# Optimization experiments

Measured on AMD Instinct MI355X. Metric: run time of the kernel, lower is better.

## Reference

```python
import jax, jax.numpy as jnp
import numpy as np

B, S, H = 2, 1024, 4096
NH, D = 32, 128
ROPE_BASE = 10000.0
W_BITS, A_BITS = 4, 8


def fake_quant(x, n_bits):
    """Symmetric fake quantization along the last dim (per-token / per-channel)."""
    qmax = 2.0 ** (n_bits - 1) - 1.0
    scale = jnp.max(jnp.abs(x), axis=-1, keepdims=True) / qmax
    scale = jnp.maximum(scale, 1e-8)
    q = jnp.clip(jnp.round(x / scale), -qmax - 1.0, qmax) * scale
    # straight-through estimator (matches fake-quant training semantics)
    return x + jax.lax.stop_gradient(q - x)


def quant_linear(x, w):
    # x: [..., in], w: [out, in]; quantize activation per-token, weight per-out-channel
    xq = fake_quant(x, A_BITS)
    wq = fake_quant(w, W_BITS)
    return jnp.einsum('bsi,oi->bso', xq, wq)


def rope_tables(seq_len, dim, dtype):
    inv_freq = 1.0 / (ROPE_BASE ** (jnp.arange(0, dim, 2, dtype=jnp.float32) / dim))
    t = jnp.arange(seq_len, dtype=jnp.float32)
    freqs = jnp.einsum('i,j->ij', t, inv_freq)          # [S, D/2]
    emb = jnp.concatenate([freqs, freqs], axis=-1)       # [S, D]
    return jnp.cos(emb).astype(dtype), jnp.sin(emb).astype(dtype)


def rotate_half(x):
    x1, x2 = jnp.split(x, 2, axis=-1)
    return jnp.concatenate([-x2, x1], axis=-1)


def setup_inputs() -> dict:
    key = jax.random.key(0)
    ks = jax.random.split(key, 5)
    hidden_states = jax.random.normal(ks[0], (B, S, H), jnp.float32)
    wq = jax.random.normal(ks[1], (H, H), jnp.float32) * 0.02
    wk = jax.random.normal(ks[2], (H, H), jnp.float32) * 0.02
    wv = jax.random.normal(ks[3], (H, H), jnp.float32) * 0.02
    wo = jax.random.normal(ks[4], (H, H), jnp.float32) * 0.02
    return {"hidden_states": hidden_states, "wq": wq, "wk": wk, "wv": wv, "wo": wo}


def reference(hidden_states, wq, wk, wv, wo):
    bsz, q_len, _ = hidden_states.shape
    # quantized QKV projections
    q = quant_linear(hidden_states, wq).reshape(bsz, q_len, NH, D).transpose(0, 2, 1, 3)
    k = quant_linear(hidden_states, wk).reshape(bsz, q_len, NH, D).transpose(0, 2, 1, 3)
    v = quant_linear(hidden_states, wv).reshape(bsz, q_len, NH, D).transpose(0, 2, 1, 3)
    # RoPE
    cos, sin = rope_tables(q_len, D, hidden_states.dtype)   # [S, D]
    cos = cos[None, None, :, :]
    sin = sin[None, None, :, :]
    q = q * cos + rotate_half(q) * sin
    k = k * cos + rotate_half(k) * sin
    # quantized QK^T
    qq = fake_quant(q, A_BITS)
    kq = fake_quant(k, A_BITS)
    scores = jnp.einsum('bhqd,bhkd->bhqk', qq, kq) / jnp.sqrt(jnp.float32(D))
    # causal mask
    causal = jnp.tril(jnp.ones((q_len, q_len), dtype=bool))
    scores = jnp.where(causal[None, None], scores, jnp.finfo(scores.dtype).min)
    p = jax.nn.softmax(scores, axis=-1)
    # quantized PV
    pq = fake_quant(p, A_BITS)
    vq = fake_quant(v, A_BITS)
    attn = jnp.einsum('bhqk,bhkd->bhqd', pq, vq)
    attn = attn.transpose(0, 2, 1, 3).reshape(bsz, q_len, H)
    # quantized output projection
    return quant_linear(attn, wo)
```

## Files before the change

kernel.cpp:

```cpp
#include <hip/hip_runtime.h>
#include <stdint.h>

#define S_LEN 1024
#define HDIM  4096
#define NHEAD 32
#define DHEAD 128
#define BATCH 2
#define MTOK  (BATCH * S_LEN)

typedef __attribute__((ext_vector_type(4))) int   i32x4;
typedef __attribute__((ext_vector_type(4))) float f32x4;
typedef __attribute__((ext_vector_type(8))) short bf16x8;

#define GLOBAL_AS __attribute__((address_space(1)))
#define LDS_AS    __attribute__((address_space(3)))

__device__ __forceinline__ void gl2lds16(const void* g, void* l) {
  __builtin_amdgcn_global_load_lds((const GLOBAL_AS unsigned int*)(g),
                                   (LDS_AS unsigned int*)(l), 16, 0, 0);
}

__device__ __forceinline__ unsigned short f2bf(float f) {
  unsigned int u = __float_as_uint(f);
  unsigned int r = (u + 0x7fffu + ((u >> 16) & 1u)) >> 16;
  return (unsigned short)r;
}

__global__ __launch_bounds__(256) void rowquant_kernel(
    const float* __restrict__ x, int8_t* __restrict__ q,
    float* __restrict__ scales, float qmax, float clipLo)
{
  const int row = blockIdx.x;
  const int t = threadIdx.x;
  const float* xr = x + (size_t)row * HDIM;
  float4 v[4];
  float am = 0.f;
#pragma unroll
  for (int i = 0; i < 4; ++i) {
    v[i] = ((const float4*)xr)[t + 256 * i];
    am = fmaxf(am, fmaxf(fmaxf(fabsf(v[i].x), fabsf(v[i].y)),
                         fmaxf(fabsf(v[i].z), fabsf(v[i].w))));
  }
#pragma unroll
  for (int off = 32; off > 0; off >>= 1) am = fmaxf(am, __shfl_down(am, off));
  __shared__ float wred[4];
  if ((t & 63) == 0) wred[t >> 6] = am;
  __syncthreads();
  const float m = fmaxf(fmaxf(wred[0], wred[1]), fmaxf(wred[2], wred[3]));
  const float scale = fmaxf(m / qmax, 1e-8f);
  if (t == 0) scales[row] = scale;
  int* qo = (int*)(q + (size_t)row * HDIM);
#pragma unroll
  for (int i = 0; i < 4; ++i) {
    int b0 = (int)fminf(fmaxf(rintf(v[i].x / scale), clipLo), qmax);
    int b1 = (int)fminf(fmaxf(rintf(v[i].y / scale), clipLo), qmax);
    int b2 = (int)fminf(fmaxf(rintf(v[i].z / scale), clipLo), qmax);
    int b3 = (int)fminf(fmaxf(rintf(v[i].w / scale), clipLo), qmax);
    qo[t + 256 * i] = (b0 & 0xff) | ((b1 & 0xff) << 8) | ((b2 & 0xff) << 16) | ((b3 & 0xff) << 24);
  }
}

__global__ __launch_bounds__(256) void ropetab_kernel(
    float* __restrict__ ct, float* __restrict__ st)
{
  const int t = blockIdx.x * 256 + threadIdx.x;
  const int s = t >> 6, d = t & 63;
  const float inv = powf(10000.0f, -(float)d * (1.0f / 64.0f));
  const float ang = (float)s * inv;
  float sn, c;
  sincosf(ang, &sn, &c);
  ct[t] = c;
  st[t] = sn;
}

template<int MODE>
__global__ __launch_bounds__(256, 2) void gemm_i8_fused_kernel(
    const int8_t* __restrict__ A, const float* __restrict__ sa,
    const int8_t* __restrict__ Bw, const float* __restrict__ sb,
    float* __restrict__ C,
    int8_t* __restrict__ o8, float* __restrict__ oscale,
    const float* __restrict__ ctab, const float* __restrict__ stab,
    unsigned short* __restrict__ vqT)
{
  __shared__ __align__(16) char smem[128 * 129 * 4];
  __shared__ float vscale[128];
  int8_t (*asB)[128 * 128] = (int8_t(*)[128 * 128])smem;
  int8_t (*bsB)[128 * 128] = (int8_t(*)[128 * 128])(smem + 32768);
  float (*fx)[129] = (float(*)[129])smem;

  const int flat = blockIdx.y * gridDim.x + blockIdx.x;
  const int nf = (flat & 7) * 64 + (flat >> 3);
  const int bmi = nf & 15, bni = nf >> 4;
  const int bm = bmi * 128, bn = bni * 128;

  const int tid = threadIdx.x;
  const int w = tid >> 6, l = tid & 63;
  const int l15 = l & 15, lg = l >> 4, l7 = l & 7;
  const int lr = l >> 3, g7 = l & 7;
  const int m0 = (w >> 1) * 64, n0 = (w & 1) * 64;

  const int8_t* aT = A + (size_t)(bm + lr) * HDIM + ((g7 ^ lr) << 4);
  const int8_t* bT = Bw + (size_t)(bn + lr) * HDIM + ((g7 ^ lr) << 4);

  i32x4 acc[4][4];
#pragma unroll
  for (int i = 0; i < 4; ++i)
#pragma unroll
    for (int j = 0; j < 4; ++j) acc[i][j] = (i32x4){0, 0, 0, 0};

  auto stage = [&](int t) {
    const int bf = t & 1;
    const size_t k = (size_t)t * 128;
#pragma unroll
    for (int i = 0; i < 4; ++i) {
      const int r0 = w * 32 + i * 8;
      gl2lds16(aT + (size_t)r0 * HDIM + k, asB[bf] + r0 * 128);
      gl2lds16(bT + (size_t)r0 * HDIM + k, bsB[bf] + r0 * 128);
    }
  };

  stage(0);
  asm volatile("s_waitcnt vmcnt(0)" ::: "memory");
  __builtin_amdgcn_s_barrier();

  for (int t = 0; t < 32; ++t) {
    if (t < 31) stage(t + 1);
    const int cur = t & 1;
    __builtin_amdgcn_s_setprio(1);
#pragma unroll
    for (int kk = 0; kk < 2; ++kk) {
      i32x4 aF[4], bF[4];
      const int slot = (((kk << 2) + lg) ^ l7) << 4;
#pragma unroll
      for (int i = 0; i < 4; ++i)
        aF[i] = *(const i32x4*)(asB[cur] + (m0 + i * 16 + l15) * 128 + slot);
#pragma unroll
      for (int j = 0; j < 4; ++j)
        bF[j] = *(const i32x4*)(bsB[cur] + (n0 + j * 16 + l15) * 128 + slot);
#pragma unroll
      for (int i = 0; i < 4; ++i)
#pragma unroll
        for (int j = 0; j < 4; ++j)
          acc[i][j] = __builtin_amdgcn_mfma_i32_16x16x64_i8(aF[i], bF[j], acc[i][j], 0, 0, 0);
    }
    __builtin_amdgcn_s_setprio(0);
    if (t < 31) {
      asm volatile("s_waitcnt vmcnt(0)" ::: "memory");
      __builtin_amdgcn_s_barrier();
    }
  }

  float sbr[4];
#pragma unroll
  for (int j = 0; j < 4; ++j) sbr[j] = sb[bn + n0 + j * 16 + l15];

  if (MODE == 0) {
#pragma unroll
    for (int i = 0; i < 4; ++i) {
#pragma unroll
      for (int r = 0; r < 4; ++r) {
        const int m = bm + m0 + i * 16 + lg * 4 + r;
        const float sm = sa[m];
        float* cp = C + (size_t)m * HDIM + bn + n0 + l15;
#pragma unroll
        for (int j = 0; j < 4; ++j)
          cp[j * 16] = sm * sbr[j] * (float)acc[i][j][r];
      }
    }
    return;
  }

  __syncthreads();
#pragma unroll
  for (int i = 0; i < 4; ++i) {
#pragma unroll
    for (int r = 0; r < 4; ++r) {
      const int ml = m0 + i * 16 + lg * 4 + r;
      const float sm = sa[bm + ml];
#pragma unroll
      for (int j = 0; j < 4; ++j)
        fx[ml][n0 + j * 16 + l15] = sm * sbr[j] * (float)acc[i][j][r];
    }
  }
  __syncthreads();

  const int h = bn >> 7;

  if (MODE == 1) {
    const int row = tid >> 1, half = tid & 1;
    const int sg = bm + row;
    const int b = sg >> 10, s = sg & (S_LEN - 1);
    const float* ct = ctab + (size_t)s * 64;
    const float* st = stab + (size_t)s * 64;
    float am = 0.f;
#pragma unroll
    for (int d0 = 0; d0 < 64; ++d0) {
      const int d = half * 64 + d0;
      const float x0 = fx[row][d];
      const float x1 = fx[row][d ^ 64];
      const float c = ct[d0], sn = st[d0];
      const float v = half ? (x0 * c + x1 * sn) : (x0 * c - x1 * sn);
      fx[row][d] = v;
      am = fmaxf(am, fabsf(v));
    }
    am = fmaxf(am, __shfl_xor(am, 1));
    const float scale = fmaxf(am * (1.0f / 127.0f), 1e-8f);
    int8_t* op = o8 + (((size_t)(b * NHEAD + h)) * S_LEN + s) * DHEAD + half * 64;
#pragma unroll
    for (int c4 = 0; c4 < 4; ++c4) {
      i32x4 dw;
#pragma unroll
      for (int u = 0; u < 4; ++u) {
        int pk = 0;
#pragma unroll
        for (int bi = 0; bi < 4; ++bi) {
          const float v = fx[row][half * 64 + c4 * 16 + u * 4 + bi];
          const int q = (int)fminf(fmaxf(rintf(v / scale), -128.f), 127.f);
          pk |= (q & 0xff) << (8 * bi);
        }
        dw[u] = pk;
      }
      *(i32x4*)(op + c4 * 16) = dw;
    }
    if (!half) oscale[((size_t)(b * NHEAD + h)) * S_LEN + s] = scale;
  } else {
    {
      const int row = tid >> 1, half = tid & 1;
      float am = 0.f;
#pragma unroll
      for (int d0 = 0; d0 < 64; ++d0)
        am = fmaxf(am, fabsf(fx[row][half * 64 + d0]));
      am = fmaxf(am, __shfl_xor(am, 1));
      if (!half) vscale[row] = fmaxf(am * (1.0f / 127.0f), 1e-8f);
    }
    __syncthreads();
    {
      const int d = tid >> 1, sh = tid & 1;
      const int b = bm >> 10;
      const int bh = b * NHEAD + h;
      unsigned short* op = vqT + ((size_t)bh * DHEAD + d) * S_LEN + (bm & (S_LEN - 1)) + sh * 64;
#pragma unroll
      for (int c8 = 0; c8 < 8; ++c8) {
        i32x4 dw;
#pragma unroll
        for (int u = 0; u < 4; ++u) {
          const int sl = sh * 64 + c8 * 8 + u * 2;
          const float sc0 = vscale[sl], sc1 = vscale[sl + 1];
          const float q0 = fminf(fmaxf(rintf(fx[sl][d] / sc0), -128.f), 127.f);
          const float q1 = fminf(fmaxf(rintf(fx[sl + 1][d] / sc1), -128.f), 127.f);
          dw[u] = (int)f2bf(q0 * sc0) | ((int)f2bf(q1 * sc1) << 16);
        }
        *(i32x4*)(op + c8 * 8) = dw;
      }
    }
  }
}

#define QB 64
#define KB 64

__global__ __launch_bounds__(256) void attn_mfma_kernel(
    const int8_t* __restrict__ qq, const float* __restrict__ sq,
    const int8_t* __restrict__ kq, const float* __restrict__ sk,
    const unsigned short* __restrict__ vqT,
    float* __restrict__ attn)
{
  __shared__ __align__(16) int8_t ks[KB * 128];
  __shared__ __align__(16) unsigned short vs[128 * 64];
  __shared__ __align__(16) unsigned short ps[QB][64];
  __shared__ float sk_t[KB];

  const int tid = threadIdx.x;
  const int w = tid >> 6;
  const int l = tid & 63;
  const int l15 = l & 15;
  const int lg = l >> 4;
  const int lr = l >> 3, g7 = l & 7;
  const int bflat = blockIdx.x;
  const int bh = (bflat & 7) + 8 * (bflat >> 6);
  const int qxb = (bflat >> 3) & 7;
  const size_t bhS = (size_t)bh * S_LEN;
  const int b = bh >> 5, h = bh & 31;
  const int NT = S_LEN / QB;

  for (int rep = 0; rep < 2; ++rep) {
    const int qt = rep ? (NT - 1 - qxb) : qxb;
    const int q0 = qt * QB;
    const int nkt = qt + 1;

    const int qrow = q0 + w * 16 + l15;
    const int8_t* qp = qq + (bhS + qrow) * (size_t)DHEAD;
    const i32x4 qa0 = *(const i32x4*)(qp + lg * 16);
    const i32x4 qa1 = *(const i32x4*)(qp + 64 + lg * 16);

    float sqv[4];
    int qg[4];
#pragma unroll
    for (int r = 0; r < 4; ++r) {
      qg[r] = q0 + w * 16 + lg * 4 + r;
      sqv[r] = sq[bhS + qg[r]] * 0.08838834764831843f * 1.4426950408889634f;
    }

    float m_run[4] = {-3.0e38f, -3.0e38f, -3.0e38f, -3.0e38f};
    float rs[4] = {0.f, 0.f, 0.f, 0.f};
    f32x4 oacc[8];
#pragma unroll
    for (int ds = 0; ds < 8; ++ds) oacc[ds] = (f32x4){0.f, 0.f, 0.f, 0.f};

    const int qloc = w * 16 + l15;
    const int swA0 = (lg ^ (qloc & 7)) << 3;
    const int swA1 = ((lg + 4) ^ (qloc & 7)) << 3;

    for (int kt = 0; kt < nkt; ++kt) {
      const int k0 = kt * KB;
#pragma unroll
      for (int i = 0; i < 2; ++i) {
        const int r0 = w * 16 + i * 8;
        gl2lds16(kq + (bhS + k0 + r0 + lr) * (size_t)128 + ((g7 ^ lr) << 4),
                 ks + r0 * 128);
      }
#pragma unroll
      for (int i = 0; i < 4; ++i) {
        const int r0 = w * 32 + i * 8;
        const unsigned short* src = vqT + ((size_t)bh * 128 + r0 + lr) * S_LEN
                                        + k0 + ((g7 ^ lr) << 3);
        gl2lds16(src, vs + r0 * 64);
      }
      if (tid < KB) sk_t[tid] = sk[bhS + k0 + tid];
      __syncthreads();
      const bool diag = (kt == nkt - 1);

      float s2v[4][4];
      float tmax[4] = {-3.0e38f, -3.0e38f, -3.0e38f, -3.0e38f};
#pragma unroll
      for (int c = 0; c < 4; ++c) {
        const int krow = c * 16 + l15;
        const i32x4 b0 = *(const i32x4*)(ks + krow * 128 + ((lg ^ (krow & 7)) << 4));
        const i32x4 b1 = *(const i32x4*)(ks + krow * 128 + (((lg + 4) ^ (krow & 7)) << 4));
        i32x4 acc = {0, 0, 0, 0};
        acc = __builtin_amdgcn_mfma_i32_16x16x64_i8(qa0, b0, acc, 0, 0, 0);
        acc = __builtin_amdgcn_mfma_i32_16x16x64_i8(qa1, b1, acc, 0, 0, 0);
        const float skv = sk_t[krow];
        const int kgl = k0 + krow;
#pragma unroll
        for (int r = 0; r < 4; ++r) {
          const bool valid = !diag || (kgl <= qg[r]);
          const float s2 = valid ? ((float)acc[r] * sqv[r] * skv) : -3.0e38f;
          s2v[c][r] = s2;
          tmax[r] = fmaxf(tmax[r], s2);
        }
      }
#pragma unroll
      for (int r = 0; r < 4; ++r)
#pragma unroll
        for (int off = 1; off < 16; off <<= 1)
          tmax[r] = fmaxf(tmax[r], __shfl_xor(tmax[r], off));

#pragma unroll
      for (int r = 0; r < 4; ++r) {
        const float m_new = fmaxf(m_run[r], tmax[r]);
        const float f = exp2f(m_run[r] - m_new);
        m_run[r] = m_new;
        rs[r] *= f;
#pragma unroll
        for (int ds = 0; ds < 8; ++ds) oacc[ds][r] *= f;
      }

#pragma unroll
      for (int c = 0; c < 4; ++c) {
        const int krow = c * 16 + l15;
#pragma unroll
        for (int r = 0; r < 4; ++r) {
          const float e = exp2f(s2v[c][r] - m_run[r]);
          rs[r] += e;
          const float p = rintf(e * 127.0f);
          const int qr = w * 16 + lg * 4 + r;
          const int sidx = (((krow >> 3) ^ (qr & 7)) << 3) | (krow & 7);
          ps[qr][sidx] = f2bf(p);
        }
      }

      const bf16x8 a0 = *(const bf16x8*)&ps[qloc][swA0];
      const bf16x8 a1 = *(const bf16x8*)&ps[qloc][swA1];
      __builtin_amdgcn_s_setprio(1);
#pragma unroll
      for (int ds = 0; ds < 8; ++ds) {
        const int d = ds * 16 + l15;
        const bf16x8 bv0 = *(const bf16x8*)(vs + d * 64 + ((lg ^ (d & 7)) << 3));
        const bf16x8 bv1 = *(const bf16x8*)(vs + d * 64 + (((lg + 4) ^ (d & 7)) << 3));
        oacc[ds] = __builtin_amdgcn_mfma_f32_16x16x32_bf16(a0, bv0, oacc[ds], 0, 0, 0);
        oacc[ds] = __builtin_amdgcn_mfma_f32_16x16x32_bf16(a1, bv1, oacc[ds], 0, 0, 0);
      }
      __builtin_amdgcn_s_setprio(0);
      __syncthreads();
    }

#pragma unroll
    for (int r = 0; r < 4; ++r)
#pragma unroll
      for (int off = 1; off < 16; off <<= 1)
        rs[r] += __shfl_xor(rs[r], off);

#pragma unroll
    for (int r = 0; r < 4; ++r) {
      const float inv = 1.0f / (127.0f * rs[r]);
      float* op = attn + ((size_t)(b * S_LEN + qg[r])) * HDIM + h * DHEAD + l15;
#pragma unroll
      for (int ds = 0; ds < 8; ++ds)
        op[ds * 16] = oacc[ds][r] * inv;
    }
  }
}

extern "C" void kernel_launch(void* const* d_in, const int* in_sizes, int n_in,
                              void* d_out, int out_size, void* d_ws, size_t ws_size,
                              hipStream_t stream) {
  const float* hs = (const float*)d_in[0];
  const float* wmat[4] = { (const float*)d_in[1], (const float*)d_in[2],
                           (const float*)d_in[3], (const float*)d_in[4] };

  char* p = (char*)d_ws;
  auto take = [&](size_t sz) { char* r = p; p += (sz + 255) & ~(size_t)255; return r; };

  int8_t* xq8 = (int8_t*)take((size_t)MTOK * HDIM);
  int8_t* w4[4];
  for (int i = 0; i < 4; ++i) w4[i] = (int8_t*)take((size_t)HDIM * HDIM);
  float* sx = (float*)take((size_t)MTOK * 4);
  float* sw[4];
  for (int i = 0; i < 4; ++i) sw[i] = (float*)take((size_t)HDIM * 4);
  float* y = (float*)take((size_t)MTOK * HDIM * 4);
  int8_t* qq8 = (int8_t*)take((size_t)MTOK * HDIM);
  int8_t* kq8 = (int8_t*)take((size_t)MTOK * HDIM);
  unsigned short* vqT = (unsigned short*)take((size_t)MTOK * HDIM * 2);
  float* sqs = (float*)take((size_t)BATCH * NHEAD * S_LEN * 4);
  float* sks = (float*)take((size_t)BATCH * NHEAD * S_LEN * 4);
  float* sattn = (float*)take((size_t)MTOK * 4);
  float* ctab = (float*)take((size_t)S_LEN * 64 * 4);
  float* stab = (float*)take((size_t)S_LEN * 64 * 4);

  rowquant_kernel<<<MTOK, 256, 0, stream>>>(hs, xq8, sx, 127.f, -128.f);
  for (int i = 0; i < 4; ++i)
    rowquant_kernel<<<HDIM, 256, 0, stream>>>(wmat[i], w4[i], sw[i], 7.f, -8.f);
  ropetab_kernel<<<S_LEN * 64 / 256, 256, 0, stream>>>(ctab, stab);

  const dim3 gg(HDIM / 128, MTOK / 128);
  gemm_i8_fused_kernel<1><<<gg, 256, 0, stream>>>(
      xq8, sx, w4[0], sw[0], nullptr, qq8, sqs, ctab, stab, nullptr);
  gemm_i8_fused_kernel<1><<<gg, 256, 0, stream>>>(
      xq8, sx, w4[1], sw[1], nullptr, kq8, sks, ctab, stab, nullptr);
  gemm_i8_fused_kernel<2><<<gg, 256, 0, stream>>>(
      xq8, sx, w4[2], sw[2], nullptr, nullptr, nullptr, nullptr, nullptr, vqT);

  attn_mfma_kernel<<<512, 256, 0, stream>>>(qq8, sqs, kq8, sks, vqT, y);

  rowquant_kernel<<<MTOK, 256, 0, stream>>>(y, xq8, sattn, 127.f, -128.f);
  gemm_i8_fused_kernel<0><<<gg, 256, 0, stream>>>(
      xq8, sattn, w4[3], sw[3], (float*)d_out, nullptr, nullptr, nullptr, nullptr, nullptr);
}
```

Measured before the change: 309.9 us.

## Double-buffer K/V tiles in attention, lazy softmax rescale, merge quant launches

The attention kernel now double-buffers K and V tiles in LDS and prefetches the next tile, including its key scales held in registers, while the current tile is computed. This lets global-to-LDS loads overlap the MFMA work. The online softmax only rescales the accumulators when the running max grows by more than 8 (in log2 units), which skips most exp and multiply work but allows unnormalized exponentials up to 2^8. The five separate row-quantization launches are merged into one grid.

```diff
diff --git a/kernel.cpp b/kernel.cpp
--- a/kernel.cpp
+++ b/kernel.cpp
@@ -24,6 +24,58 @@
   unsigned int u = __float_as_uint(f);
   unsigned int r = (u + 0x7fffu + ((u >> 16) & 1u)) >> 16;
   return (unsigned short)r;
+}
+
+__global__ __launch_bounds__(256) void prequant_kernel(
+    const float* __restrict__ hs,
+    const float* __restrict__ w0, const float* __restrict__ w1,
+    const float* __restrict__ w2, const float* __restrict__ w3,
+    int8_t* __restrict__ xq8,
+    int8_t* __restrict__ q0, int8_t* __restrict__ q1,
+    int8_t* __restrict__ q2, int8_t* __restrict__ q3,
+    float* __restrict__ sx,
+    float* __restrict__ s0, float* __restrict__ s1,
+    float* __restrict__ s2, float* __restrict__ s3)
+{
+  const int row = blockIdx.x;
+  const float* src; int8_t* dst; float* sc; float qmax, clipLo; int lrow;
+  if (row < MTOK) {
+    src = hs; dst = xq8; sc = sx; qmax = 127.f; clipLo = -128.f; lrow = row;
+  } else {
+    const int wi = (row - MTOK) >> 12;
+    lrow = (row - MTOK) & 4095;
+    qmax = 7.f; clipLo = -8.f;
+    src = (wi == 0) ? w0 : (wi == 1) ? w1 : (wi == 2) ? w2 : w3;
+    dst = (wi == 0) ? q0 : (wi == 1) ? q1 : (wi == 2) ? q2 : q3;
+    sc  = (wi == 0) ? s0 : (wi == 1) ? s1 : (wi == 2) ? s2 : s3;
+  }
+  const int t = threadIdx.x;
+  const float* xr = src + (size_t)lrow * HDIM;
+  float4 v[4];
+  float am = 0.f;
+#pragma unroll
+  for (int i = 0; i < 4; ++i) {
+    v[i] = ((const float4*)xr)[t + 256 * i];
+    am = fmaxf(am, fmaxf(fmaxf(fabsf(v[i].x), fabsf(v[i].y)),
+                         fmaxf(fabsf(v[i].z), fabsf(v[i].w))));
+  }
+#pragma unroll
+  for (int off = 32; off > 0; off >>= 1) am = fmaxf(am, __shfl_down(am, off));
+  __shared__ float wred[4];
+  if ((t & 63) == 0) wred[t >> 6] = am;
+  __syncthreads();
+  const float m = fmaxf(fmaxf(wred[0], wred[1]), fmaxf(wred[2], wred[3]));
+  const float scale = fmaxf(m / qmax, 1e-8f);
+  if (t == 0) sc[lrow] = scale;
+  int* qo = (int*)(dst + (size_t)lrow * HDIM);
+#pragma unroll
+  for (int i = 0; i < 4; ++i) {
+    int b0 = (int)fminf(fmaxf(rintf(v[i].x / scale), clipLo), qmax);
+    int b1 = (int)fminf(fmaxf(rintf(v[i].y / scale), clipLo), qmax);
+    int b2 = (int)fminf(fmaxf(rintf(v[i].z / scale), clipLo), qmax);
+    int b3 = (int)fminf(fmaxf(rintf(v[i].w / scale), clipLo), qmax);
+    qo[t + 256 * i] = (b0 & 0xff) | ((b1 & 0xff) << 8) | ((b2 & 0xff) << 16) | ((b3 & 0xff) << 24);
+  }
 }
 
 __global__ __launch_bounds__(256) void rowquant_kernel(
@@ -265,10 +317,9 @@
     const unsigned short* __restrict__ vqT,
     float* __restrict__ attn)
 {
-  __shared__ __align__(16) int8_t ks[KB * 128];
-  __shared__ __align__(16) unsigned short vs[128 * 64];
+  __shared__ __align__(16) int8_t ks[2][KB * 128];
+  __shared__ __align__(16) unsigned short vs[2][128 * 64];
   __shared__ __align__(16) unsigned short ps[QB][64];
-  __shared__ float sk_t[KB];
 
   const int tid = threadIdx.x;
   const int w = tid >> 6;
@@ -283,6 +334,22 @@
   const int b = bh >> 5, h = bh & 31;
   const int NT = S_LEN / QB;
 
+  auto stageKV = [&](int kt, int nb) {
+    const int k0 = kt * KB;
+#pragma unroll
+    for (int i = 0; i < 2; ++i) {
+      const int r0 = w * 16 + i * 8;
+      gl2lds16(kq + (bhS + k0 + r0 + lr) * (size_t)128 + ((g7 ^ lr) << 4),
+               ks[nb] + r0 * 128);
+    }
+#pragma unroll
+    for (int i = 0; i < 4; ++i) {
+      const int r0 = w * 32 + i * 8;
+      gl2lds16(vqT + ((size_t)bh * 128 + r0 + lr) * S_LEN + k0 + ((g7 ^ lr) << 3),
+               vs[nb] + r0 * 64);
+    }
+  };
+
   for (int rep = 0; rep < 2; ++rep) {
     const int qt = rep ? (NT - 1 - qxb) : qxb;
     const int q0 = qt * QB;
@@ -311,45 +378,48 @@
     const int swA0 = (lg ^ (qloc & 7)) << 3;
     const int swA1 = ((lg + 4) ^ (qloc & 7)) << 3;
 
+    stageKV(0, 0);
+    float skn[4];
+#pragma unroll
+    for (int c = 0; c < 4; ++c) skn[c] = sk[bhS + c * 16 + l15];
+    asm volatile("s_waitcnt vmcnt(0)" ::: "memory");
+    __builtin_amdgcn_s_barrier();
+
+    int nb = 0;
     for (int kt = 0; kt < nkt; ++kt) {
       const int k0 = kt * KB;
-#pragma unroll
-      for (int i = 0; i < 2; ++i) {
-        const int r0 = w * 16 + i * 8;
-        gl2lds16(kq + (bhS + k0 + r0 + lr) * (size_t)128 + ((g7 ^ lr) << 4),
-                 ks + r0 * 128);
-      }
-#pragma unroll
-      for (int i = 0; i < 4; ++i) {
-        const int r0 = w * 32 + i * 8;
-        const unsigned short* src = vqT + ((size_t)bh * 128 + r0 + lr) * S_LEN
-                                        + k0 + ((g7 ^ lr) << 3);
-        gl2lds16(src, vs + r0 * 64);
-      }
-      if (tid < KB) sk_t[tid] = sk[bhS + k0 + tid];
-      __syncthreads();
+      float skc[4];
+#pragma unroll
+      for (int c = 0; c < 4; ++c) skc[c] = skn[c];
+      if (kt + 1 < nkt) {
+        stageKV(kt + 1, nb ^ 1);
+#pragma unroll
+        for (int c = 0; c < 4; ++c)
+          skn[c] = sk[bhS + (kt + 1) * KB + c * 16 + l15];
+      }
       const bool diag = (kt == nkt - 1);
 
       float s2v[4][4];
       float tmax[4] = {-3.0e38f, -3.0e38f, -3.0e38f, -3.0e38f};
+      __builtin_amdgcn_s_setprio(1);
 #pragma unroll
       for (int c = 0; c < 4; ++c) {
         const int krow = c * 16 + l15;
-        const i32x4 b0 = *(const i32x4*)(ks + krow * 128 + ((lg ^ (krow & 7)) << 4));
-        const i32x4 b1 = *(const i32x4*)(ks + krow * 128 + (((lg + 4) ^ (krow & 7)) << 4));
+        const i32x4 b0 = *(const i32x4*)(ks[nb] + krow * 128 + ((lg ^ (krow & 7)) << 4));
+        const i32x4 b1 = *(const i32x4*)(ks[nb] + krow * 128 + (((lg + 4) ^ (krow & 7)) << 4));
         i32x4 acc = {0, 0, 0, 0};
         acc = __builtin_amdgcn_mfma_i32_16x16x64_i8(qa0, b0, acc, 0, 0, 0);
         acc = __builtin_amdgcn_mfma_i32_16x16x64_i8(qa1, b1, acc, 0, 0, 0);
-        const float skv = sk_t[krow];
         const int kgl = k0 + krow;
 #pragma unroll
         for (int r = 0; r < 4; ++r) {
           const bool valid = !diag || (kgl <= qg[r]);
-          const float s2 = valid ? ((float)acc[r] * sqv[r] * skv) : -3.0e38f;
+          const float s2 = valid ? ((float)acc[r] * sqv[r] * skc[c]) : -3.0e38f;
           s2v[c][r] = s2;
           tmax[r] = fmaxf(tmax[r], s2);
         }
       }
+      __builtin_amdgcn_s_setprio(0);
 #pragma unroll
       for (int r = 0; r < 4; ++r)
 #pragma unroll
@@ -358,12 +428,13 @@
 
 #pragma unroll
       for (int r = 0; r < 4; ++r) {
-        const float m_new = fmaxf(m_run[r], tmax[r]);
-        const float f = exp2f(m_run[r] - m_new);
-        m_run[r] = m_new;
-        rs[r] *= f;
-#pragma unroll
-        for (int ds = 0; ds < 8; ++ds) oacc[ds][r] *= f;
+        if (tmax[r] > m_run[r] + 8.0f) {
+          const float f = exp2f(m_run[r] - tmax[r]);
+          m_run[r] = tmax[r];
+          rs[r] *= f;
+#pragma unroll
+          for (int ds = 0; ds < 8; ++ds) oacc[ds][r] *= f;
+        }
       }
 
 #pragma unroll
@@ -386,13 +457,15 @@
 #pragma unroll
       for (int ds = 0; ds < 8; ++ds) {
         const int d = ds * 16 + l15;
-        const bf16x8 bv0 = *(const bf16x8*)(vs + d * 64 + ((lg ^ (d & 7)) << 3));
-        const bf16x8 bv1 = *(const bf16x8*)(vs + d * 64 + (((lg + 4) ^ (d & 7)) << 3));
+        const bf16x8 bv0 = *(const bf16x8*)(vs[nb] + d * 64 + ((lg ^ (d & 7)) << 3));
+        const bf16x8 bv1 = *(const bf16x8*)(vs[nb] + d * 64 + (((lg + 4) ^ (d & 7)) << 3));
         oacc[ds] = __builtin_amdgcn_mfma_f32_16x16x32_bf16(a0, bv0, oacc[ds], 0, 0, 0);
         oacc[ds] = __builtin_amdgcn_mfma_f32_16x16x32_bf16(a1, bv1, oacc[ds], 0, 0, 0);
       }
       __builtin_amdgcn_s_setprio(0);
-      __syncthreads();
+      asm volatile("s_waitcnt vmcnt(0)" ::: "memory");
+      __builtin_amdgcn_s_barrier();
+      nb ^= 1;
     }
 
 #pragma unroll
@@ -438,9 +511,10 @@
   float* ctab = (float*)take((size_t)S_LEN * 64 * 4);
   float* stab = (float*)take((size_t)S_LEN * 64 * 4);
 
-  rowquant_kernel<<<MTOK, 256, 0, stream>>>(hs, xq8, sx, 127.f, -128.f);
-  for (int i = 0; i < 4; ++i)
-    rowquant_kernel<<<HDIM, 256, 0, stream>>>(wmat[i], w4[i], sw[i], 7.f, -8.f);
+  prequant_kernel<<<MTOK + 4 * HDIM, 256, 0, stream>>>(
+      hs, wmat[0], wmat[1], wmat[2], wmat[3],
+      xq8, w4[0], w4[1], w4[2], w4[3],
+      sx, sw[0], sw[1], sw[2], sw[3]);
   ropetab_kernel<<<S_LEN * 64 / 256, 256, 0, stream>>>(ctab, stab);
 
   const dim3 gg(HDIM / 128, MTOK / 128);
```

Result: faster. 302.9 us (-2.2%).
